# Kernel tuning notes

Hardware: AMD Instinct MI355X
Metric: run time of the kernel (lower is better)

The kernel has to match this reference:

```python
import jax, jax.numpy as jnp
import numpy as np

B, N, D, H = 4, 2048, 1024, 16
DH = D // H


def setup_inputs() -> dict:
    key = jax.random.key(0)
    ks = jax.random.split(key, 9)
    s = 1.0 / np.sqrt(D)
    return {
        "x": jax.random.normal(ks[0], (B, N, D), dtype=jnp.float32),
        "Wq": jax.random.normal(ks[1], (D, D), dtype=jnp.float32) * s,
        "bq": jax.random.normal(ks[2], (D,), dtype=jnp.float32) * 0.01,
        "Wk": jax.random.normal(ks[3], (D, D), dtype=jnp.float32) * s,
        "bk": jax.random.normal(ks[4], (D,), dtype=jnp.float32) * 0.01,
        "Wv": jax.random.normal(ks[5], (D, D), dtype=jnp.float32) * s,
        "bv": jax.random.normal(ks[6], (D,), dtype=jnp.float32) * 0.01,
        "Wp": jax.random.normal(ks[7], (D, D), dtype=jnp.float32) * s,
        "bp": jax.random.normal(ks[8], (D,), dtype=jnp.float32) * 0.01,
    }


def reference(x, Wq, bq, Wk, bk, Wv, bv, Wp, bp):
    b, n, d = x.shape
    # torch Linear: x @ W.T + b; reshape to (b, h, n, dh)
    def heads(W, bias):
        y = jnp.einsum('bnd,ed->bne', x, W) + bias
        return y.reshape(b, n, H, DH).transpose(0, 2, 1, 3)
    q, k, v = heads(Wq, bq), heads(Wk, bk), heads(Wv, bv)
    # NOTE: source multiplies by sqrt(d_head) (bug in original), kept faithfully
    scale = jnp.sqrt(jnp.float32(DH))
    att = jnp.einsum('bhqd,bhkd->bhqk', q, k) * scale
    causal = jnp.triu(jnp.ones((n, n), dtype=bool), k=1)  # True above diagonal
    att = jnp.where(causal, -jnp.inf, att)
    att = jax.nn.softmax(att, axis=-1)
    # dropout is eval-mode identity
    out = jnp.einsum('bhqk,bhkd->bhqd', att, v)
    out = out.transpose(0, 2, 1, 3).reshape(b, n, d)
    return jnp.einsum('bnd,ed->bne', out, Wp) + bp
```

## Files before the change

kernel.cpp:

```cpp
#include <hip/hip_runtime.h>
#include <hip/hip_fp16.h>


typedef _Float16 half8 __attribute__((ext_vector_type(8)));
typedef _Float16 half4 __attribute__((ext_vector_type(4)));
typedef float f32x4 __attribute__((ext_vector_type(4)));
typedef unsigned int u32x2 __attribute__((ext_vector_type(2)));

#define DEV __device__ __forceinline__
#define MFMA16(a, b, c) __builtin_amdgcn_mfma_f32_16x16x32_f16(a, b, c, 0, 0, 0)

DEV void gload_lds16(const void* g, void* l) {
  __builtin_amdgcn_global_load_lds(
      (const __attribute__((address_space(1))) void*)g,
      (__attribute__((address_space(3))) void*)l, 16, 0, 0);
}

__global__ __launch_bounds__(256) void cast_all(
    const float* __restrict__ x, const float* __restrict__ Wq,
    const float* __restrict__ Wk, const float* __restrict__ Wv,
    const float* __restrict__ Wp, __half* __restrict__ xb,
    __half* __restrict__ wqkv, __half* __restrict__ wpb) {
  int i = blockIdx.x * 256 + threadIdx.x;
  const float* s;
  __half* d;
  int j;
  if (i < 1048576) {
    s = x; d = xb; j = i;
  } else {
    int k = i - 1048576;
    int sel = k >> 17;
    j = k & 131071;
    s = (sel == 0) ? Wq : (sel == 1) ? Wk : (sel == 2) ? Wv : Wp;
    d = (sel == 3) ? wpb : (wqkv + sel * 1048576);
  }
  const float4* sp = (const float4*)s + (size_t)j * 2;
  float4 a = sp[0], b = sp[1];
  half8 h;
  h[0] = (_Float16)a.x; h[1] = (_Float16)a.y; h[2] = (_Float16)a.z; h[3] = (_Float16)a.w;
  h[4] = (_Float16)b.x; h[5] = (_Float16)b.y; h[6] = (_Float16)b.z; h[7] = (_Float16)b.w;
  *((half8*)d + j) = h;
}

template <int MODE>
__global__ __launch_bounds__(256) void gemm128(
    const __half* __restrict__ A, const __half* __restrict__ Bm,
    const float* __restrict__ b0, const float* __restrict__ b1,
    const float* __restrict__ b2, __half* __restrict__ oh,
    __half* __restrict__ vtp, float* __restrict__ of) {
  const int m0 = blockIdx.y * 128;
  const int n0 = blockIdx.x * 128;
  const int tid = threadIdx.x;
  const int w = tid >> 6, lane = tid & 63;
  const int lr = lane & 15, lq = lane >> 4;
  const int wr = w >> 1, wc = w & 1;

  __shared__ alignas(16) __half As[128 * 64];
  __shared__ alignas(16) __half Bs[128 * 64];

  f32x4 acc[4][4] = {};

  const int arow = lane >> 3;
  const int acol = ((lane & 7) ^ arow) * 8;
  const __half* Agp = A + ((size_t)m0 + w * 32 + arow) * 1024 + acol;
  const __half* Bgp = Bm + ((size_t)n0 + w * 32 + arow) * 1024 + acol;

  for (int kt = 0; kt < 16; ++kt) {
#pragma unroll
    for (int j = 0; j < 4; ++j) {
      gload_lds16(Agp + j * 8192 + kt * 64, As + (w * 4 + j) * 512);
      gload_lds16(Bgp + j * 8192 + kt * 64, Bs + (w * 4 + j) * 512);
    }
    __syncthreads();
#pragma unroll
    for (int s = 0; s < 2; ++s) {
      half8 af[4], bf[4];
#pragma unroll
      for (int i = 0; i < 4; ++i) {
        int rowA = wr * 64 + i * 16 + lr;
        int rowB = wc * 64 + i * 16 + lr;
        af[i] = *(const half8*)((const char*)As +
                                ((rowA * 128 + s * 64 + lq * 16) ^ ((rowA & 7) << 4)));
        bf[i] = *(const half8*)((const char*)Bs +
                                ((rowB * 128 + s * 64 + lq * 16) ^ ((rowB & 7) << 4)));
      }
#pragma unroll
      for (int mi = 0; mi < 4; ++mi)
#pragma unroll
        for (int ni = 0; ni < 4; ++ni)
          acc[mi][ni] = MFMA16(af[mi], bf[ni], acc[mi][ni]);
    }
    __syncthreads();
  }

  if (MODE == 0) {
#pragma unroll
    for (int ni = 0; ni < 4; ++ni) {
      int col = n0 + wc * 64 + ni * 16 + lr;
      int t = col >> 10, e = col & 1023;
      const float* bb = (t == 0) ? b0 : ((t == 1) ? b1 : b2);
      float bias = bb[e];
      int hh = e >> 6, dh = e & 63;
      if (t == 2) {
#pragma unroll
        for (int mi = 0; mi < 4; ++mi) {
          int row = m0 + wr * 64 + mi * 16 + lq * 4;
          int b_ = row >> 11, n = row & 2047;
          half4 h;
#pragma unroll
          for (int r = 0; r < 4; ++r) h[r] = (_Float16)(acc[mi][ni][r] + bias);
          *(half4*)(vtp + (size_t)(b_ * 16 + hh) * 131072 + (size_t)dh * 2048 + n) = h;
        }
      } else {
        float scale = (t == 0) ? 11.541560327111707f : 1.0f;
        __half* base = oh + (size_t)t * 8388608 + dh;
#pragma unroll
        for (int mi = 0; mi < 4; ++mi)
#pragma unroll
          for (int r = 0; r < 4; ++r) {
            int row = m0 + wr * 64 + mi * 16 + lq * 4 + r;
            int b_ = row >> 11, n = row & 2047;
            float v = (acc[mi][ni][r] + bias) * scale;
            base[(((size_t)(b_ * 16 + hh) * 2048 + n) * 64)] = __float2half(v);
          }
      }
    }
  } else {
#pragma unroll
    for (int ni = 0; ni < 4; ++ni) {
      int col = n0 + wc * 64 + ni * 16 + lr;
      float bias = b0[col];
#pragma unroll
      for (int mi = 0; mi < 4; ++mi)
#pragma unroll
        for (int r = 0; r < 4; ++r) {
          int row = m0 + wr * 64 + mi * 16 + lq * 4 + r;
          of[(size_t)row * 1024 + col] = acc[mi][ni][r] + bias;
        }
    }
  }
}

__global__ __launch_bounds__(256, 3) void attn128(const __half* __restrict__ Q,
                                                  const __half* __restrict__ K,
                                                  const __half* __restrict__ Vt,
                                                  __half* __restrict__ O) {
  const int wg = blockIdx.x;
  const int bh = wg & 63;
  const int qt = 15 - (wg >> 6);
  const int b = bh >> 4, h = bh & 15;
  const int tid = threadIdx.x;
  const int w = tid >> 6, lane = tid & 63;
  const int lr = lane & 15, lq = lane >> 4;

  __shared__ alignas(16) __half Ks[2][4096];
  __shared__ alignas(16) __half Vs[2][4096];
  __shared__ alignas(16) unsigned Pl[4][512];

  const __half* Kb = K + (size_t)bh * 131072;
  const __half* Vb = Vt + (size_t)bh * 131072;

  const int srow0 = tid >> 3;
  const int srow1 = srow0 + 32;
  const int scol = ((tid & 7) ^ (srow0 & 7)) * 8;

#define STAGE(t, buf)                                                          \
  do {                                                                         \
    gload_lds16(Kb + (size_t)((t)*64 + srow0) * 64 + scol, Ks[buf] + tid * 8); \
    gload_lds16(Kb + (size_t)((t)*64 + srow1) * 64 + scol,                     \
                Ks[buf] + 2048 + tid * 8);                                     \
    gload_lds16(Vb + (size_t)srow0 * 2048 + (t)*64 + scol, Vs[buf] + tid * 8); \
    gload_lds16(Vb + (size_t)srow1 * 2048 + (t)*64 + scol,                     \
                Vs[buf] + 2048 + tid * 8);                                     \
  } while (0)

  const int q0 = qt * 128;
  const int ktend = 2 * qt + 2;
  const int rmin = q0 + w * 32;
  const int myqa = rmin + lr;
  const int myqb = rmin + 16 + lr;

  const __half* Qpa = Q + ((size_t)bh * 2048 + rmin) * 64;
  half8 qf0a = *(const half8*)(Qpa + lr * 64 + lq * 8);
  half8 qf1a = *(const half8*)(Qpa + lr * 64 + 32 + lq * 8);
  half8 qf0b = *(const half8*)(Qpa + (16 + lr) * 64 + lq * 8);
  half8 qf1b = *(const half8*)(Qpa + (16 + lr) * 64 + 32 + lq * 8);

  f32x4 oacca[4] = {}, oaccb[4] = {};
  float ma = -INFINITY, la = 0.f, mb = -INFINITY, lb = 0.f;

  STAGE(0, 0);
  asm volatile("" ::: "memory");

  char* Pc = (char*)Pl[w];

  auto smgrp = [&](f32x4* sacc, float& m, float& l, int myq, int k0,
                   bool needmask, f32x4* oacc, half8& pa0, half8& pa1) {
    if (needmask) {
#pragma unroll
      for (int nt = 0; nt < 4; ++nt)
#pragma unroll
        for (int r = 0; r < 4; ++r) {
          int key = k0 + nt * 16 + lq * 4 + r;
          if (key > myq) sacc[nt][r] = -INFINITY;
        }
    }
    float rm = fmaxf(sacc[0][0], sacc[0][1]);
    rm = fmaxf(fmaxf(rm, sacc[0][2]), sacc[0][3]);
    rm = fmaxf(fmaxf(rm, sacc[1][0]), sacc[1][1]);
    rm = fmaxf(fmaxf(rm, sacc[1][2]), sacc[1][3]);
    rm = fmaxf(fmaxf(rm, sacc[2][0]), sacc[2][1]);
    rm = fmaxf(fmaxf(rm, sacc[2][2]), sacc[2][3]);
    rm = fmaxf(fmaxf(rm, sacc[3][0]), sacc[3][1]);
    rm = fmaxf(fmaxf(rm, sacc[3][2]), sacc[3][3]);
    rm = fmaxf(rm, __shfl_xor(rm, 16));
    rm = fmaxf(rm, __shfl_xor(rm, 32));
    if (__any(rm > m + 8.f)) {
      float mn = fmaxf(m, rm);
      float al = __builtin_amdgcn_exp2f(m - mn);
      m = mn;
      l *= al;
      float al4[4];
#pragma unroll
      for (int r = 0; r < 4; ++r) al4[r] = __shfl(al, lq * 4 + r);
#pragma unroll
      for (int dt = 0; dt < 4; ++dt)
#pragma unroll
        for (int r = 0; r < 4; ++r) oacc[dt][r] *= al4[r];
    }
    float ps = 0.f;
#pragma unroll
    for (int nt = 0; nt < 4; ++nt) {
      float p0 = __builtin_amdgcn_exp2f(sacc[nt][0] - m);
      float p1 = __builtin_amdgcn_exp2f(sacc[nt][1] - m);
      float p2 = __builtin_amdgcn_exp2f(sacc[nt][2] - m);
      float p3 = __builtin_amdgcn_exp2f(sacc[nt][3] - m);
      sacc[nt][0] = p0; sacc[nt][1] = p1;
      sacc[nt][2] = p2; sacc[nt][3] = p3;
      ps += (p0 + p1) + (p2 + p3);
    }
    l += ps;
#pragma unroll
    for (int nt = 0; nt < 4; ++nt) {
      __half2 pha = __floats2half2_rn(sacc[nt][0], sacc[nt][1]);
      __half2 phb = __floats2half2_rn(sacc[nt][2], sacc[nt][3]);
      u32x2 pw;
      pw[0] = *(unsigned*)&pha;
      pw[1] = *(unsigned*)&phb;
      *(u32x2*)(Pc + ((lr * 128 + nt * 32 + lq * 8) ^ ((lr & 7) << 4))) = pw;
    }
    pa0 = *(const half8*)(Pc + ((lr * 128 + lq * 16) ^ ((lr & 7) << 4)));
    pa1 = *(const half8*)(Pc + ((lr * 128 + 64 + lq * 16) ^ ((lr & 7) << 4)));
  };

  for (int kt = 0; kt < ktend; ++kt) {
    const int cur = kt & 1;
    const int k0 = kt * 64;
    if (kt + 1 < ktend) {
      STAGE(kt + 1, cur ^ 1);
      asm volatile("s_waitcnt vmcnt(4)" ::: "memory");
    } else {
      asm volatile("s_waitcnt vmcnt(0)" ::: "memory");
    }
    __builtin_amdgcn_s_barrier();
    asm volatile("" ::: "memory");

    const char* Kc = (const char*)Ks[cur];
    const char* Vc = (const char*)Vs[cur];
    if (k0 <= rmin + 31) {
      f32x4 sa[4] = {}, sb[4] = {};
      __builtin_amdgcn_s_setprio(1);
#pragma unroll
      for (int nt = 0; nt < 4; ++nt) {
        int row = nt * 16 + lr;
        half8 kb0 = *(const half8*)(Kc + ((row * 128 + lq * 16) ^ ((row & 7) << 4)));
        half8 kb1 = *(const half8*)(Kc + ((row * 128 + 64 + lq * 16) ^ ((row & 7) << 4)));
        sa[nt] = MFMA16(kb0, qf0a, sa[nt]);
        sa[nt] = MFMA16(kb1, qf1a, sa[nt]);
        sb[nt] = MFMA16(kb0, qf0b, sb[nt]);
        sb[nt] = MFMA16(kb1, qf1b, sb[nt]);
      }
      __builtin_amdgcn_s_setprio(0);

      half8 paa0, paa1, pab0, pab1;
      smgrp(sa, ma, la, myqa, k0, k0 + 63 > rmin, oacca, paa0, paa1);
      smgrp(sb, mb, lb, myqb, k0, k0 + 63 > rmin + 16, oaccb, pab0, pab1);

      __builtin_amdgcn_s_setprio(1);
#pragma unroll
      for (int dt = 0; dt < 4; ++dt) {
        int row = dt * 16 + lr;
        half8 vb0 = *(const half8*)(Vc + ((row * 128 + lq * 16) ^ ((row & 7) << 4)));
        half8 vb1 = *(const half8*)(Vc + ((row * 128 + 64 + lq * 16) ^ ((row & 7) << 4)));
        oacca[dt] = MFMA16(paa0, vb0, oacca[dt]);
        oacca[dt] = MFMA16(paa1, vb1, oacca[dt]);
        oaccb[dt] = MFMA16(pab0, vb0, oaccb[dt]);
        oaccb[dt] = MFMA16(pab1, vb1, oaccb[dt]);
      }
      __builtin_amdgcn_s_setprio(0);
    }
    asm volatile("s_waitcnt lgkmcnt(0)" ::: "memory");
    __builtin_amdgcn_s_barrier();
    asm volatile("" ::: "memory");
  }

  auto epi = [&](f32x4* oacc, float lpart, int grow) {
    float lt = lpart;
    lt += __shfl_xor(lt, 16);
    lt += __shfl_xor(lt, 32);
    float linv = 1.0f / lt;
    float inv4[4];
#pragma unroll
    for (int r = 0; r < 4; ++r) inv4[r] = __shfl(linv, lq * 4 + r);
    __half* Op = O + ((size_t)b * 2048 + rmin + grow) * 1024 + h * 64;
#pragma unroll
    for (int dt = 0; dt < 4; ++dt)
#pragma unroll
      for (int r = 0; r < 4; ++r)
        Op[(size_t)(lq * 4 + r) * 1024 + dt * 16 + lr] =
            __float2half(oacc[dt][r] * inv4[r]);
  };
  epi(oacca, la, 0);
  epi(oaccb, lb, 16);
#undef STAGE
}

extern "C" void kernel_launch(void* const* d_in, const int* in_sizes, int n_in,
                              void* d_out, int out_size, void* d_ws,
                              size_t ws_size, hipStream_t stream) {
  const float* x = (const float*)d_in[0];
  const float* Wq = (const float*)d_in[1];
  const float* bq = (const float*)d_in[2];
  const float* Wk = (const float*)d_in[3];
  const float* bk = (const float*)d_in[4];
  const float* Wv = (const float*)d_in[5];
  const float* bv = (const float*)d_in[6];
  const float* Wp = (const float*)d_in[7];
  const float* bp = (const float*)d_in[8];

  char* ws = (char*)d_ws;
  const size_t XB = 0;
  const size_t WQKV = XB + 16777216;
  const size_t WPB = WQKV + 6291456;
  const size_t QKV = WPB + 2097152;
  const size_t VT = QKV + 50331648;
  const size_t OB = VT + 16777216;

  __half* xb = (__half*)(ws + XB);
  __half* wqkv = (__half*)(ws + WQKV);
  __half* wpb = (__half*)(ws + WPB);
  __half* qkv = (__half*)(ws + QKV);
  __half* vt = (__half*)(ws + VT);
  __half* ob = (__half*)(ws + OB);

  cast_all<<<6144, 256, 0, stream>>>(x, Wq, Wk, Wv, Wp, xb, wqkv, wpb);

  gemm128<0><<<dim3(24, 64), 256, 0, stream>>>(xb, wqkv, bq, bk, bv, qkv, vt,
                                               nullptr);
  attn128<<<dim3(1024), 256, 0, stream>>>(qkv, qkv + 8388608, vt, ob);
  gemm128<1><<<dim3(8, 64), 256, 0, stream>>>(ob, wpb, bp, nullptr, nullptr,
                                              nullptr, nullptr, (float*)d_out);
}
```

Before: 173.2 us.

## Use 256x192 double-buffered tile for QKV projection GEMM

Replaces the 128x128 QKV projection GEMM with a 512-thread kernel using 256x192 tiles. It adds double-buffered LDS staging via direct global-to-LDS loads, with explicit vmcnt waits so the next k-tile's loads overlap the current tile's MFMAs. The larger tile raises arithmetic intensity and cuts the grid to 512 blocks, which is meant to reduce global traffic and keep the matrix units busy. The costs are heavier register and LDS use (about 112KB of LDS per block) and possible occupancy or wave-quantization effects on 256 CUs. The output projection GEMM is split out unchanged as its own kernel.

```diff
diff --git a/kernel.cpp b/kernel.cpp
--- a/kernel.cpp
+++ b/kernel.cpp
@@ -42,12 +42,117 @@
   *((half8*)d + j) = h;
 }
 
-template <int MODE>
-__global__ __launch_bounds__(256) void gemm128(
+__global__ __launch_bounds__(512, 2) void gemm256(
     const __half* __restrict__ A, const __half* __restrict__ Bm,
     const float* __restrict__ b0, const float* __restrict__ b1,
     const float* __restrict__ b2, __half* __restrict__ oh,
-    __half* __restrict__ vtp, float* __restrict__ of) {
+    __half* __restrict__ vtp) {
+  const int m0 = blockIdx.y * 256;
+  const int n0 = blockIdx.x * 192;
+  const int tid = threadIdx.x;
+  const int w = tid >> 6, lane = tid & 63;
+  const int lr = lane & 15, lq = lane >> 4;
+  const int wr = w >> 2, wc = w & 3;
+
+  __shared__ alignas(16) __half As[2][16384];
+  __shared__ alignas(16) __half Bs[2][12288];
+
+  f32x4 acc[8][3] = {};
+
+  const int srow = tid >> 3;
+  const int scol = ((tid & 7) ^ (srow & 7)) * 8;
+  const __half* Agp = A + ((size_t)m0 + srow) * 1024 + scol;
+  const __half* Bgp = Bm + ((size_t)n0 + srow) * 1024 + scol;
+
+#define STG(kt, buf)                                                           \
+  do {                                                                         \
+    const __half* ag = Agp + (kt)*64;                                          \
+    const __half* bg = Bgp + (kt)*64;                                          \
+    gload_lds16(ag, As[buf] + tid * 8);                                        \
+    gload_lds16(ag + 65536, As[buf] + 4096 + tid * 8);                         \
+    gload_lds16(ag + 131072, As[buf] + 8192 + tid * 8);                        \
+    gload_lds16(ag + 196608, As[buf] + 12288 + tid * 8);                       \
+    gload_lds16(bg, Bs[buf] + tid * 8);                                        \
+    gload_lds16(bg + 65536, Bs[buf] + 4096 + tid * 8);                         \
+    gload_lds16(bg + 131072, Bs[buf] + 8192 + tid * 8);                        \
+  } while (0)
+
+  STG(0, 0);
+  STG(1, 1);
+  asm volatile("" ::: "memory");
+
+  for (int kt = 0; kt < 16; ++kt) {
+    const int s = kt & 1;
+    if (kt < 15) asm volatile("s_waitcnt vmcnt(7)" ::: "memory");
+    else         asm volatile("s_waitcnt vmcnt(0)" ::: "memory");
+    __builtin_amdgcn_s_barrier();
+    asm volatile("" ::: "memory");
+
+    const char* Ac = (const char*)As[s];
+    const char* Bc = (const char*)Bs[s];
+    __builtin_amdgcn_s_setprio(1);
+#pragma unroll
+    for (int ks = 0; ks < 2; ++ks) {
+      half8 bf[3];
+#pragma unroll
+      for (int ni = 0; ni < 3; ++ni) {
+        int row = wc * 48 + ni * 16 + lr;
+        bf[ni] = *(const half8*)(Bc + ((row * 128 + ks * 64 + lq * 16) ^ ((row & 7) << 4)));
+      }
+#pragma unroll
+      for (int mi = 0; mi < 8; ++mi) {
+        int row = wr * 128 + mi * 16 + lr;
+        half8 af = *(const half8*)(Ac + ((row * 128 + ks * 64 + lq * 16) ^ ((row & 7) << 4)));
+        acc[mi][0] = MFMA16(af, bf[0], acc[mi][0]);
+        acc[mi][1] = MFMA16(af, bf[1], acc[mi][1]);
+        acc[mi][2] = MFMA16(af, bf[2], acc[mi][2]);
+      }
+    }
+    __builtin_amdgcn_s_setprio(0);
+
+    asm volatile("s_waitcnt lgkmcnt(0)" ::: "memory");
+    __builtin_amdgcn_s_barrier();
+    asm volatile("" ::: "memory");
+    if (kt + 2 < 16) STG(kt + 2, s);
+  }
+
+#pragma unroll
+  for (int ni = 0; ni < 3; ++ni) {
+    int col = n0 + wc * 48 + ni * 16 + lr;
+    int t = col >> 10, e = col & 1023;
+    const float* bb = (t == 0) ? b0 : ((t == 1) ? b1 : b2);
+    float bias = bb[e];
+    int hh = e >> 6, dh = e & 63;
+    if (t == 2) {
+#pragma unroll
+      for (int mi = 0; mi < 8; ++mi) {
+        int row = m0 + wr * 128 + mi * 16 + lq * 4;
+        int b_ = row >> 11, n = row & 2047;
+        half4 h;
+#pragma unroll
+        for (int r = 0; r < 4; ++r) h[r] = (_Float16)(acc[mi][ni][r] + bias);
+        *(half4*)(vtp + (size_t)(b_ * 16 + hh) * 131072 + (size_t)dh * 2048 + n) = h;
+      }
+    } else {
+      float scale = (t == 0) ? 11.541560327111707f : 1.0f;
+      __half* base = oh + (size_t)t * 8388608 + dh;
+#pragma unroll
+      for (int mi = 0; mi < 8; ++mi)
+#pragma unroll
+        for (int r = 0; r < 4; ++r) {
+          int row = m0 + wr * 128 + mi * 16 + lq * 4 + r;
+          int b_ = row >> 11, n = row & 2047;
+          float v = (acc[mi][ni][r] + bias) * scale;
+          base[(((size_t)(b_ * 16 + hh) * 2048 + n) * 64)] = __float2half(v);
+        }
+    }
+  }
+#undef STG
+}
+
+__global__ __launch_bounds__(256) void gemm128p(
+    const __half* __restrict__ A, const __half* __restrict__ Bm,
+    const float* __restrict__ b0, float* __restrict__ of) {
   const int m0 = blockIdx.y * 128;
   const int n0 = blockIdx.x * 128;
   const int tid = threadIdx.x;
@@ -93,51 +198,17 @@
     __syncthreads();
   }
 
-  if (MODE == 0) {
-#pragma unroll
-    for (int ni = 0; ni < 4; ++ni) {
-      int col = n0 + wc * 64 + ni * 16 + lr;
-      int t = col >> 10, e = col & 1023;
-      const float* bb = (t == 0) ? b0 : ((t == 1) ? b1 : b2);
-      float bias = bb[e];
-      int hh = e >> 6, dh = e & 63;
-      if (t == 2) {
-#pragma unroll
-        for (int mi = 0; mi < 4; ++mi) {
-          int row = m0 + wr * 64 + mi * 16 + lq * 4;
-          int b_ = row >> 11, n = row & 2047;
-          half4 h;
-#pragma unroll
-          for (int r = 0; r < 4; ++r) h[r] = (_Float16)(acc[mi][ni][r] + bias);
-          *(half4*)(vtp + (size_t)(b_ * 16 + hh) * 131072 + (size_t)dh * 2048 + n) = h;
-        }
-      } else {
-        float scale = (t == 0) ? 11.541560327111707f : 1.0f;
-        __half* base = oh + (size_t)t * 8388608 + dh;
-#pragma unroll
-        for (int mi = 0; mi < 4; ++mi)
-#pragma unroll
-          for (int r = 0; r < 4; ++r) {
-            int row = m0 + wr * 64 + mi * 16 + lq * 4 + r;
-            int b_ = row >> 11, n = row & 2047;
-            float v = (acc[mi][ni][r] + bias) * scale;
-            base[(((size_t)(b_ * 16 + hh) * 2048 + n) * 64)] = __float2half(v);
-          }
-      }
-    }
-  } else {
-#pragma unroll
-    for (int ni = 0; ni < 4; ++ni) {
-      int col = n0 + wc * 64 + ni * 16 + lr;
-      float bias = b0[col];
-#pragma unroll
-      for (int mi = 0; mi < 4; ++mi)
-#pragma unroll
-        for (int r = 0; r < 4; ++r) {
-          int row = m0 + wr * 64 + mi * 16 + lq * 4 + r;
-          of[(size_t)row * 1024 + col] = acc[mi][ni][r] + bias;
-        }
-    }
+#pragma unroll
+  for (int ni = 0; ni < 4; ++ni) {
+    int col = n0 + wc * 64 + ni * 16 + lr;
+    float bias = b0[col];
+#pragma unroll
+    for (int mi = 0; mi < 4; ++mi)
+#pragma unroll
+      for (int r = 0; r < 4; ++r) {
+        int row = m0 + wr * 64 + mi * 16 + lq * 4 + r;
+        of[(size_t)row * 1024 + col] = acc[mi][ni][r] + bias;
+      }
   }
 }
 
@@ -355,9 +426,7 @@
 
   cast_all<<<6144, 256, 0, stream>>>(x, Wq, Wk, Wv, Wp, xb, wqkv, wpb);
 
-  gemm128<0><<<dim3(24, 64), 256, 0, stream>>>(xb, wqkv, bq, bk, bv, qkv, vt,
-                                               nullptr);
+  gemm256<<<dim3(16, 32), 512, 0, stream>>>(xb, wqkv, bq, bk, bv, qkv, vt);
   attn128<<<dim3(1024), 256, 0, stream>>>(qkv, qkv + 8388608, vt, ob);
-  gemm128<1><<<dim3(8, 64), 256, 0, stream>>>(ob, wpb, bp, nullptr, nullptr,
-                                              nullptr, nullptr, (float*)d_out);
-}
+  gemm128p<<<dim3(8, 64), 256, 0, stream>>>(ob, wpb, bp, (float*)d_out);
+}
```

Result: no change. 170.6 us (-1.5%).

## Replace QKV GEMM with 256x192-tile double-buffered pipelined kernel

Applied to the files above, without the earlier changes.

Adds a dedicated QKV projection kernel using 512-thread blocks with 256x192 output tiles and double-buffered LDS. Loads for the next k-tile are split into four chunks interleaved with the MFMA clusters, and setprio raises wave priority during the math. The goal is to hide global-load latency and increase per-block reuse, with 512 blocks instead of 1536. The trade-off is higher LDS and register use per block and more barriers per k-step. The output GEMM stays as before.

```diff
diff --git a/kernel.cpp b/kernel.cpp
--- a/kernel.cpp
+++ b/kernel.cpp
@@ -42,12 +42,161 @@
   *((half8*)d + j) = h;
 }
 
-template <int MODE>
-__global__ __launch_bounds__(256) void gemm128(
+__global__ __launch_bounds__(512, 2) void gemmQKV(
     const __half* __restrict__ A, const __half* __restrict__ Bm,
     const float* __restrict__ b0, const float* __restrict__ b1,
     const float* __restrict__ b2, __half* __restrict__ oh,
-    __half* __restrict__ vtp, float* __restrict__ of) {
+    __half* __restrict__ vtp) {
+  const int m0 = blockIdx.y * 256;
+  const int n0 = blockIdx.x * 192;
+  const int tid = threadIdx.x;
+  const int w = tid >> 6, lane = tid & 63;
+  const int lr = lane & 15, lq = lane >> 4;
+  const int wr = w >> 2, wc = w & 3;
+
+  __shared__ alignas(16) __half As[2][16384];
+  __shared__ alignas(16) __half Bs[2][12288];
+
+  f32x4 acc[2][4][3] = {};
+
+  const int srow = tid >> 3;
+  const int scol = ((tid & 7) ^ (srow & 7)) * 8;
+  const __half* Agp = A + ((size_t)m0 + srow) * 1024 + scol;
+  const __half* Bgp = Bm + ((size_t)n0 + srow) * 1024 + scol;
+
+#define SPAIR(T, BUF, P)                                                       \
+  do {                                                                         \
+    if ((P) == 0) {                                                            \
+      gload_lds16(Agp + (T)*64, As[BUF] + tid * 8);                            \
+      gload_lds16(Agp + (T)*64 + 65536, As[BUF] + 4096 + tid * 8);             \
+    } else if ((P) == 1) {                                                     \
+      gload_lds16(Agp + (T)*64 + 131072, As[BUF] + 8192 + tid * 8);            \
+      gload_lds16(Agp + (T)*64 + 196608, As[BUF] + 12288 + tid * 8);           \
+    } else if ((P) == 2) {                                                     \
+      gload_lds16(Bgp + (T)*64, Bs[BUF] + tid * 8);                            \
+      gload_lds16(Bgp + (T)*64 + 65536, Bs[BUF] + 4096 + tid * 8);             \
+    } else {                                                                   \
+      gload_lds16(Bgp + (T)*64 + 131072, Bs[BUF] + 8192 + tid * 8);            \
+    }                                                                          \
+  } while (0)
+
+#define RD_A(af, Ac, mh, ks)                                                   \
+  do {                                                                         \
+    _Pragma("unroll") for (int mi = 0; mi < 4; ++mi) {                         \
+      int row = wr * 128 + (mh)*64 + mi * 16 + lr;                             \
+      af[mi] = *(const half8*)((Ac) +                                          \
+                               ((row * 128 + (ks)*64 + lq * 16) ^ ((row & 7) << 4))); \
+    }                                                                          \
+  } while (0)
+
+#define RD_B(bf, Bc, ks)                                                       \
+  do {                                                                         \
+    _Pragma("unroll") for (int ni = 0; ni < 3; ++ni) {                         \
+      int row = wc * 48 + ni * 16 + lr;                                        \
+      bf[ni] = *(const half8*)((Bc) +                                          \
+                               ((row * 128 + (ks)*64 + lq * 16) ^ ((row & 7) << 4))); \
+    }                                                                          \
+  } while (0)
+
+#define CLUSTER(mh, af, bf)                                                    \
+  do {                                                                         \
+    __builtin_amdgcn_s_setprio(1);                                             \
+    _Pragma("unroll") for (int mi = 0; mi < 4; ++mi) {                         \
+      acc[mh][mi][0] = MFMA16(af[mi], bf[0], acc[mh][mi][0]);                  \
+      acc[mh][mi][1] = MFMA16(af[mi], bf[1], acc[mh][mi][1]);                  \
+      acc[mh][mi][2] = MFMA16(af[mi], bf[2], acc[mh][mi][2]);                  \
+    }                                                                          \
+    __builtin_amdgcn_s_setprio(0);                                             \
+  } while (0)
+
+#define BAR()                                                                  \
+  do {                                                                         \
+    asm volatile("" ::: "memory");                                             \
+    __builtin_amdgcn_s_barrier();                                              \
+    asm volatile("" ::: "memory");                                             \
+  } while (0)
+
+  SPAIR(0, 0, 0);
+  SPAIR(0, 0, 1);
+  SPAIR(0, 0, 2);
+  SPAIR(0, 0, 3);
+  asm volatile("" ::: "memory");
+
+  for (int t = 0; t < 16; ++t) {
+    const int s = t & 1;
+    const char* Ac = (const char*)As[s];
+    const char* Bc = (const char*)Bs[s];
+    half8 af[4], bf0[3], bf1[3];
+
+    if (t < 15) {
+      SPAIR(t + 1, s ^ 1, 0);
+      asm volatile("s_waitcnt vmcnt(2)" ::: "memory");
+    } else {
+      asm volatile("s_waitcnt vmcnt(0)" ::: "memory");
+    }
+    BAR();
+    RD_B(bf0, Bc, 0);
+    RD_A(af, Ac, 0, 0);
+    CLUSTER(0, af, bf0);
+    BAR();
+    RD_A(af, Ac, 1, 0);
+    if (t < 15) SPAIR(t + 1, s ^ 1, 1);
+    CLUSTER(1, af, bf0);
+    BAR();
+    RD_B(bf1, Bc, 1);
+    RD_A(af, Ac, 0, 1);
+    if (t < 15) SPAIR(t + 1, s ^ 1, 2);
+    CLUSTER(0, af, bf1);
+    BAR();
+    RD_A(af, Ac, 1, 1);
+    if (t < 15) SPAIR(t + 1, s ^ 1, 3);
+    CLUSTER(1, af, bf1);
+    BAR();
+  }
+
+#pragma unroll
+  for (int mh = 0; mh < 2; ++mh)
+#pragma unroll
+    for (int ni = 0; ni < 3; ++ni) {
+      int col = n0 + wc * 48 + ni * 16 + lr;
+      int t = col >> 10, e = col & 1023;
+      const float* bb = (t == 0) ? b0 : ((t == 1) ? b1 : b2);
+      float bias = bb[e];
+      int hh = e >> 6, dh = e & 63;
+      if (t == 2) {
+#pragma unroll
+        for (int mi = 0; mi < 4; ++mi) {
+          int row = m0 + wr * 128 + mh * 64 + mi * 16 + lq * 4;
+          int b_ = row >> 11, n = row & 2047;
+          half4 h;
+#pragma unroll
+          for (int r = 0; r < 4; ++r) h[r] = (_Float16)(acc[mh][mi][ni][r] + bias);
+          *(half4*)(vtp + (size_t)(b_ * 16 + hh) * 131072 + (size_t)dh * 2048 + n) = h;
+        }
+      } else {
+        float scale = (t == 0) ? 11.541560327111707f : 1.0f;
+        __half* base = oh + (size_t)t * 8388608 + dh;
+#pragma unroll
+        for (int mi = 0; mi < 4; ++mi)
+#pragma unroll
+          for (int r = 0; r < 4; ++r) {
+            int row = m0 + wr * 128 + mh * 64 + mi * 16 + lq * 4 + r;
+            int b_ = row >> 11, n = row & 2047;
+            float v = (acc[mh][mi][ni][r] + bias) * scale;
+            base[(((size_t)(b_ * 16 + hh) * 2048 + n) * 64)] = __float2half(v);
+          }
+      }
+    }
+#undef SPAIR
+#undef RD_A
+#undef RD_B
+#undef CLUSTER
+#undef BAR
+}
+
+__global__ __launch_bounds__(256) void gemm128p(
+    const __half* __restrict__ A, const __half* __restrict__ Bm,
+    const float* __restrict__ b0, float* __restrict__ of) {
   const int m0 = blockIdx.y * 128;
   const int n0 = blockIdx.x * 128;
   const int tid = threadIdx.x;
@@ -93,51 +242,17 @@
     __syncthreads();
   }
 
-  if (MODE == 0) {
-#pragma unroll
-    for (int ni = 0; ni < 4; ++ni) {
-      int col = n0 + wc * 64 + ni * 16 + lr;
-      int t = col >> 10, e = col & 1023;
-      const float* bb = (t == 0) ? b0 : ((t == 1) ? b1 : b2);
-      float bias = bb[e];
-      int hh = e >> 6, dh = e & 63;
-      if (t == 2) {
-#pragma unroll
-        for (int mi = 0; mi < 4; ++mi) {
-          int row = m0 + wr * 64 + mi * 16 + lq * 4;
-          int b_ = row >> 11, n = row & 2047;
-          half4 h;
-#pragma unroll
-          for (int r = 0; r < 4; ++r) h[r] = (_Float16)(acc[mi][ni][r] + bias);
-          *(half4*)(vtp + (size_t)(b_ * 16 + hh) * 131072 + (size_t)dh * 2048 + n) = h;
-        }
-      } else {
-        float scale = (t == 0) ? 11.541560327111707f : 1.0f;
-        __half* base = oh + (size_t)t * 8388608 + dh;
-#pragma unroll
-        for (int mi = 0; mi < 4; ++mi)
-#pragma unroll
-          for (int r = 0; r < 4; ++r) {
-            int row = m0 + wr * 64 + mi * 16 + lq * 4 + r;
-            int b_ = row >> 11, n = row & 2047;
-            float v = (acc[mi][ni][r] + bias) * scale;
-            base[(((size_t)(b_ * 16 + hh) * 2048 + n) * 64)] = __float2half(v);
-          }
+#pragma unroll
+  for (int ni = 0; ni < 4; ++ni) {
+    int col = n0 + wc * 64 + ni * 16 + lr;
+    float bias = b0[col];
+#pragma unroll
+    for (int mi = 0; mi < 4; ++mi)
+#pragma unroll
+      for (int r = 0; r < 4; ++r) {
+        int row = m0 + wr * 64 + mi * 16 + lq * 4 + r;
+        of[(size_t)row * 1024 + col] = acc[mi][ni][r] + bias;
       }
-    }
-  } else {
-#pragma unroll
-    for (int ni = 0; ni < 4; ++ni) {
-      int col = n0 + wc * 64 + ni * 16 + lr;
-      float bias = b0[col];
-#pragma unroll
-      for (int mi = 0; mi < 4; ++mi)
-#pragma unroll
-        for (int r = 0; r < 4; ++r) {
-          int row = m0 + wr * 64 + mi * 16 + lq * 4 + r;
-          of[(size_t)row * 1024 + col] = acc[mi][ni][r] + bias;
-        }
-    }
   }
 }
 
@@ -355,9 +470,7 @@
 
   cast_all<<<6144, 256, 0, stream>>>(x, Wq, Wk, Wv, Wp, xb, wqkv, wpb);
 
-  gemm128<0><<<dim3(24, 64), 256, 0, stream>>>(xb, wqkv, bq, bk, bv, qkv, vt,
-                                               nullptr);
+  gemmQKV<<<dim3(16, 32), 512, 0, stream>>>(xb, wqkv, bq, bk, bv, qkv, vt);
   attn128<<<dim3(1024), 256, 0, stream>>>(qkv, qkv + 8388608, vt, ob);
-  gemm128<1><<<dim3(8, 64), 256, 0, stream>>>(ob, wpb, bp, nullptr, nullptr,
-                                              nullptr, nullptr, (float*)d_out);
-}
+  gemm128p<<<dim3(8, 64), 256, 0, stream>>>(ob, wpb, bp, (float*)d_out);
+}
```

After: 167.8 us, median of 2. 1.03x faster.
